# Performance work log

Measured on AMD Instinct MI355X. Metric: run time of the kernel, lower is better.

The kernel has to match this reference:

```python
import jax, jax.numpy as jnp
import numpy as np

N_NODES = 50000
N_EDGES = 800000
IN_F = 96
HID = 64
N_CLS = 32


def setup_inputs() -> dict:
    key = jax.random.key(0)
    k1, k2, k3, k4 = jax.random.split(key, 4)
    x = jax.random.normal(k1, (N_NODES, IN_F), dtype=jnp.float32)
    edge_index = jax.random.randint(k2, (2, N_EDGES), 0, N_NODES, dtype=jnp.int64)
    # xavier_uniform init for weights, zeros for bias
    lim1 = float(np.sqrt(6.0 / (IN_F + HID)))
    lim2 = float(np.sqrt(6.0 / (HID + N_CLS)))
    W1 = jax.random.uniform(k3, (IN_F, HID), minval=-lim1, maxval=lim1, dtype=jnp.float32)
    W2 = jax.random.uniform(k4, (HID, N_CLS), minval=-lim2, maxval=lim2, dtype=jnp.float32)
    b1 = jnp.zeros((HID,), dtype=jnp.float32)
    b2 = jnp.zeros((N_CLS,), dtype=jnp.float32)
    return {"x": x, "edge_index": edge_index, "W1": W1, "b1": b1, "W2": W2, "b2": b2}


def _ghost_conv(h, src, dst, W, b, num_nodes):
    # gather neighbor feats per edge, per-edge matmul, scatter-add, bias
    msg = h[src] @ W                                   # [E, out]
    agg = jax.ops.segment_sum(msg, dst, num_segments=num_nodes)  # [N, out]
    return agg + b


def reference(x, edge_index, W1, b1, W2, b2):
    src, dst = edge_index[0], edge_index[1]
    n = x.shape[0]
    h = jax.nn.relu(_ghost_conv(x, src, dst, W1, b1, n))
    # F.dropout(training=False) is identity in eval mode
    out = _ghost_conv(h, src, dst, W2, b2, n)
    return jax.nn.log_softmax(out, axis=1)
```

## Files before the change

kernel.cpp:

```cpp
#include <hip/hip_runtime.h>
#include <hip/hip_bf16.h>
#include <hip/hip_fp8.h>

typedef __attribute__((ext_vector_type(8))) short bf16x8;
typedef __attribute__((ext_vector_type(4))) float f32x4;

#define NBLK 256
#define NBINS_PAD 800
#define BCAP 2048
#define W1LD 104
#define HLD 72

__device__ inline unsigned short f2bf(float f) {
    unsigned u = __float_as_uint(f);
    return (unsigned short)((u + 0x7fffu + ((u >> 16) & 1u)) >> 16);
}
__device__ inline unsigned pack2(float a, float b) {
    return (unsigned)f2bf(a) | ((unsigned)f2bf(b) << 16);
}
__device__ inline float blo(unsigned u) { return __uint_as_float(u << 16); }
__device__ inline float bhi(unsigned u) { return __uint_as_float(u & 0xffff0000u); }

__device__ inline void acc8(float* a, uint4 v) {
    a[0] += blo(v.x); a[1] += bhi(v.x);
    a[2] += blo(v.y); a[3] += bhi(v.y);
    a[4] += blo(v.z); a[5] += bhi(v.z);
    a[6] += blo(v.w); a[7] += bhi(v.w);
}

__device__ inline void accf8x4(float* a, unsigned u) {
    __hip_fp8_e4m3 t;
    t.__x = (__hip_fp8_storage_t)(u & 0xff);         a[0] += (float)t;
    t.__x = (__hip_fp8_storage_t)((u >> 8) & 0xff);  a[1] += (float)t;
    t.__x = (__hip_fp8_storage_t)((u >> 16) & 0xff); a[2] += (float)t;
    t.__x = (__hip_fp8_storage_t)((u >> 24) & 0xff); a[3] += (float)t;
}
__device__ inline void accf8(float* a, uint4 v) {
    accf8x4(a, v.x); accf8x4(a + 4, v.y); accf8x4(a + 8, v.z); accf8x4(a + 12, v.w);
}

__global__ __launch_bounds__(256) void fused_hist_gemm1(
        const int* __restrict__ ei, int* __restrict__ counts, int E, int chunk, int nb,
        const float* __restrict__ W1, const float* __restrict__ W2,
        unsigned short* __restrict__ w2t,
        const float* __restrict__ X,
        unsigned char* __restrict__ y1f8, int Mtiles) {
    __shared__ int hist[NBINS_PAD];
    __shared__ unsigned short w1l[64 * W1LD];
    int b = blockIdx.x, t = threadIdx.x;
    if (b < NBLK) {
        for (int i = t; i < NBINS_PAD; i += 256) hist[i] = 0;
        __syncthreads();
        int e0 = b * chunk;
        int n = E - e0; if (n > chunk) n = chunk; if (n < 0) n = 0;
        for (int i = t; i < n; i += 256) atomicAdd(&hist[ei[E + e0 + i] >> 6], 1);
        __syncthreads();
        for (int j = t; j < nb; j += 256) counts[j * NBLK + b] = hist[j];
        return;
    }
    if (b == NBLK) {
        for (int idx = t; idx < 64 * 32; idx += 256) {
            int n = idx / 64, k = idx - n * 64;
            w2t[idx] = f2bf(W2[k * 32 + n]);
        }
        return;
    }
    for (int idx = t; idx < 96 * 64; idx += 256) {
        int n = idx / 96, k = idx - n * 96;
        w1l[n * W1LD + k] = f2bf(W1[k * 64 + n]);
    }
    __syncthreads();
    int wave = (b - NBLK - 1) * 4 + (t >> 6);
    if (wave >= Mtiles) return;
    int lane = t & 63;
    int l15 = lane & 15, quad = lane >> 4;
    const float* arow = X + (long)(wave * 16 + l15) * 96 + quad * 8;
    f32x4 acc[4] = {{0,0,0,0},{0,0,0,0},{0,0,0,0},{0,0,0,0}};
#pragma unroll
    for (int tt = 0; tt < 3; ++tt) {
        float4 p0 = *(const float4*)(arow + tt * 32);
        float4 p1 = *(const float4*)(arow + tt * 32 + 4);
        union { bf16x8 v; unsigned u[4]; } a;
        a.u[0] = pack2(p0.x, p0.y); a.u[1] = pack2(p0.z, p0.w);
        a.u[2] = pack2(p1.x, p1.y); a.u[3] = pack2(p1.z, p1.w);
#pragma unroll
        for (int nt = 0; nt < 4; ++nt) {
            bf16x8 bfr = *(const bf16x8*)(w1l + (nt * 16 + l15) * W1LD + tt * 32 + quad * 8);
            acc[nt] = __builtin_amdgcn_mfma_f32_16x16x32_bf16(a.v, bfr, acc[nt], 0, 0, 0);
        }
    }
    int mbase = wave * 16 + quad * 4;
#pragma unroll
    for (int nt = 0; nt < 4; ++nt) {
        int col = nt * 16 + l15;
#pragma unroll
        for (int r = 0; r < 4; ++r) {
            __hip_fp8_e4m3 f(acc[nt][r]);
            y1f8[(long)(mbase + r) * 64 + col] = (unsigned char)f.__x;
        }
    }
}

__global__ __launch_bounds__(256) void rowscan(int* __restrict__ counts,
                                               int* __restrict__ btot, int nb) {
    int w = (blockIdx.x * 256 + threadIdx.x) >> 6;
    int lane = threadIdx.x & 63;
    if (w >= nb) return;
    int* row = counts + (size_t)w * NBLK;
    int c0 = row[lane * 4], c1 = row[lane * 4 + 1];
    int c2 = row[lane * 4 + 2], c3 = row[lane * 4 + 3];
    int sum = c0 + c1 + c2 + c3;
    int s = sum;
#pragma unroll
    for (int o = 1; o < 64; o <<= 1) {
        int tt = __shfl_up(s, o);
        if (lane >= o) s += tt;
    }
    int run = s - sum;
    row[lane * 4] = run;     run += c0;
    row[lane * 4 + 1] = run; run += c1;
    row[lane * 4 + 2] = run; run += c2;
    row[lane * 4 + 3] = run;
    if (lane == 63) btot[w] = s;
}

__global__ __launch_bounds__(256) void blk_place(const int* __restrict__ ei,
                                                 const int* __restrict__ counts,
                                                 unsigned* __restrict__ pairs,
                                                 int E, int chunk, int nb) {
    __shared__ int cur[NBINS_PAD];
    int b = blockIdx.x, t = threadIdx.x;
    for (int j = t; j < nb; j += 256) cur[j] = (j << 11) + counts[j * NBLK + b];
    __syncthreads();
    int e0 = b * chunk;
    int n = E - e0; if (n > chunk) n = chunk; if (n < 0) n = 0;
    for (int i = t; i < n; i += 256) {
        int s = ei[e0 + i], d = ei[E + e0 + i];
        int j = d >> 6;
        int pos = atomicAdd(&cur[j], 1);
        if (pos < ((j + 1) << 11))
            pairs[pos] = (unsigned)s | ((unsigned)(d & 63) << 16);
    }
}

__global__ __launch_bounds__(256) void bucket_fused(
        const unsigned* __restrict__ pairs, const int* __restrict__ btot,
        const uint4* __restrict__ y1f8,
        const float* __restrict__ b1, const unsigned short* __restrict__ w2t,
        int2* __restrict__ noderange, int* __restrict__ srcs,
        unsigned short* __restrict__ y2, int N) {
    __shared__ unsigned spk[BCAP];
    __shared__ int lsrc[BCAP];
    __shared__ int cnt64[64], cur64[64], rs[64], re[64];
    __shared__ unsigned short htile[64 * HLD];
    int b = blockIdx.x, t = threadIdx.x;
    int base = b << 11;
    int cnt = btot[b]; if (cnt > BCAP) cnt = BCAP;
    if (t < 64) cnt64[t] = 0;
    __syncthreads();
    for (int i = t; i < cnt; i += 256) {
        unsigned p = pairs[base + i];
        spk[i] = p;
        atomicAdd(&cnt64[(p >> 16) & 63], 1);
    }
    __syncthreads();
    if (t < 64) {
        int v = cnt64[t], x = v;
#pragma unroll
        for (int o = 1; o < 64; o <<= 1) {
            int y = __shfl_up(x, o);
            if (t >= o) x += y;
        }
        int excl = x - v;
        cur64[t] = excl;
        rs[t] = excl;
        re[t] = excl + v;
        int node = b * 64 + t;
        if (node < N) noderange[node] = make_int2(base + excl, base + excl + v);
    }
    __syncthreads();
    for (int i = t; i < cnt; i += 256) {
        unsigned p = spk[i];
        int pos = atomicAdd(&cur64[(p >> 16) & 63], 1);
        lsrc[pos] = (int)(p & 0xffffu);
    }
    __syncthreads();
    for (int i = t; i < cnt; i += 256) srcs[base + i] = lsrc[i];

    int dl = t >> 2, q = t & 3;
    int s0 = rs[dl], s1 = re[dl];
    float a[16];
#pragma unroll
    for (int i = 0; i < 16; ++i) a[i] = 0.f;
    const uint4* ybase = y1f8 + q;
    int e = s0;
    for (; e + 8 <= s1; e += 8) {
        uint4 u0 = ybase[(long)lsrc[e] * 4],     u1 = ybase[(long)lsrc[e + 1] * 4];
        uint4 u2 = ybase[(long)lsrc[e + 2] * 4], u3 = ybase[(long)lsrc[e + 3] * 4];
        uint4 u4 = ybase[(long)lsrc[e + 4] * 4], u5 = ybase[(long)lsrc[e + 5] * 4];
        uint4 u6 = ybase[(long)lsrc[e + 6] * 4], u7 = ybase[(long)lsrc[e + 7] * 4];
        accf8(a, u0); accf8(a, u1); accf8(a, u2); accf8(a, u3);
        accf8(a, u4); accf8(a, u5); accf8(a, u6); accf8(a, u7);
    }
    for (; e < s1; ++e) accf8(a, ybase[(long)lsrc[e] * 4]);
    {
        const float* bq = b1 + q * 16;
        float v[16];
#pragma unroll
        for (int j = 0; j < 16; ++j) v[j] = fmaxf(a[j] + bq[j], 0.f);
        uint4 o0, o1;
        o0.x = pack2(v[0], v[1]);   o0.y = pack2(v[2], v[3]);
        o0.z = pack2(v[4], v[5]);   o0.w = pack2(v[6], v[7]);
        o1.x = pack2(v[8], v[9]);   o1.y = pack2(v[10], v[11]);
        o1.z = pack2(v[12], v[13]); o1.w = pack2(v[14], v[15]);
        uint4* hp = (uint4*)(htile + dl * HLD + q * 16);
        hp[0] = o0;
        hp[1] = o1;
    }
    __syncthreads();
    int w = t >> 6, lane = t & 63;
    int l15 = lane & 15, quad = lane >> 4;
    const unsigned short* arow = htile + (w * 16 + l15) * HLD + quad * 8;
    f32x4 acc2[2] = {{0,0,0,0},{0,0,0,0}};
#pragma unroll
    for (int t2 = 0; t2 < 2; ++t2) {
        bf16x8 af = *(const bf16x8*)(arow + t2 * 32);
#pragma unroll
        for (int nt = 0; nt < 2; ++nt) {
            bf16x8 bfr = *(const bf16x8*)(w2t + (long)(nt * 16 + l15) * 64 + t2 * 32 + quad * 8);
            acc2[nt] = __builtin_amdgcn_mfma_f32_16x16x32_bf16(af, bfr, acc2[nt], 0, 0, 0);
        }
    }
    int mbase = b * 64 + w * 16 + quad * 4;
#pragma unroll
    for (int nt = 0; nt < 2; ++nt) {
        int col = nt * 16 + l15;
#pragma unroll
        for (int r = 0; r < 4; ++r) {
            int n = mbase + r;
            if (n < N) y2[(long)n * 32 + col] = f2bf(acc2[nt][r]);
        }
    }
}

__global__ void gather_lsm(const uint4* __restrict__ y2, const int2* __restrict__ rng,
                           const int* __restrict__ srcs, const float* __restrict__ bias,
                           float* __restrict__ out, int N) {
    int gid = blockIdx.x * blockDim.x + threadIdx.x;
    int n = gid >> 2;
    if (n >= N) return;
    int q = gid & 3;
    int2 r01 = rng[n];
    int s0 = r01.x, s1 = r01.y;
    float a[8];
#pragma unroll
    for (int i = 0; i < 8; ++i) a[i] = 0.f;
    const uint4* base = y2 + q;
    int e = s0;
    for (; e + 8 <= s1; e += 8) {
        uint4 u0 = base[(long)srcs[e] * 4],     u1 = base[(long)srcs[e + 1] * 4];
        uint4 u2 = base[(long)srcs[e + 2] * 4], u3 = base[(long)srcs[e + 3] * 4];
        uint4 u4 = base[(long)srcs[e + 4] * 4], u5 = base[(long)srcs[e + 5] * 4];
        uint4 u6 = base[(long)srcs[e + 6] * 4], u7 = base[(long)srcs[e + 7] * 4];
        acc8(a, u0); acc8(a, u1); acc8(a, u2); acc8(a, u3);
        acc8(a, u4); acc8(a, u5); acc8(a, u6); acc8(a, u7);
    }
    for (; e < s1; ++e) acc8(a, base[(long)srcs[e] * 4]);
    const float* bq = bias + q * 8;
    float m = -1e30f;
#pragma unroll
    for (int i = 0; i < 8; ++i) { a[i] += bq[i]; m = fmaxf(m, a[i]); }
    m = fmaxf(m, __shfl_xor(m, 1));
    m = fmaxf(m, __shfl_xor(m, 2));
    float s = 0.f;
#pragma unroll
    for (int i = 0; i < 8; ++i) s += __expf(a[i] - m);
    s += __shfl_xor(s, 1);
    s += __shfl_xor(s, 2);
    float ls = m + __logf(s);
    float* op = out + (long)n * 32 + q * 8;
#pragma unroll
    for (int i = 0; i < 8; ++i) op[i] = a[i] - ls;
}

extern "C" void kernel_launch(void* const* d_in, const int* in_sizes, int n_in,
                              void* d_out, int out_size, void* d_ws, size_t ws_size,
                              hipStream_t stream) {
    const float* x  = (const float*)d_in[0];
    const int*   ei = (const int*)d_in[1];
    const float* W1 = (const float*)d_in[2];
    const float* b1 = (const float*)d_in[3];
    const float* W2 = (const float*)d_in[4];
    const float* b2 = (const float*)d_in[5];
    float* out = (float*)d_out;

    const int N = in_sizes[0] / 96;
    const int E = in_sizes[1] / 2;
    const int nb = (N + 63) / 64;
    const int chunk = (E + NBLK - 1) / NBLK;

    char* p = (char*)d_ws;
    unsigned char*  y1f8 = (unsigned char*)p;     p += (size_t)N * 64;
    unsigned short* y2   = (unsigned short*)p;    p += (size_t)N * 32 * 2;
    unsigned short* w2t  = (unsigned short*)p;    p += 64 * 32 * 2;
    int2* noderange = (int2*)p;                   p += (size_t)N * 8;
    int* counts = (int*)p;                        p += ((size_t)nb * NBLK * 4 + 12) & ~15ull;
    int* btot   = (int*)p;                        p += ((size_t)nb * 4 + 12) & ~15ull;
    unsigned* pairs = (unsigned*)p;               p += (size_t)nb * BCAP * 4;
    int* srcs   = (int*)p;                        p += (size_t)nb * BCAP * 4;

    const int Mtiles = N / 16;
    const int gblocks = (Mtiles + 3) / 4;

    fused_hist_gemm1<<<NBLK + 1 + gblocks, 256, 0, stream>>>(
        ei, counts, E, chunk, nb, W1, W2, w2t, x, y1f8, Mtiles);
    rowscan<<<(nb * 64 + 255) / 256, 256, 0, stream>>>(counts, btot, nb);
    blk_place<<<NBLK, 256, 0, stream>>>(ei, counts, pairs, E, chunk, nb);
    bucket_fused<<<nb, 256, 0, stream>>>(pairs, btot, (const uint4*)y1f8,
                                         b1, w2t, noderange, srcs, y2, N);
    gather_lsm<<<(N * 4 + 255) / 256, 256, 0, stream>>>(
        (const uint4*)y2, noderange, srcs, b2, out, N);
}
```

Measured before the change: 142.1 us.

## Fuse all GNN stages into one cooperative persistent kernel with grid syncs

Adds a single cooperative kernel that runs histogram plus GEMM1, row scan, edge placement, bucketed layer-1 aggregation with GEMM2, and layer-2 gather with log-softmax, separated by grid-wide syncs. One block per 64-node bucket replaces the five separate launches. The final stage reuses the per-bucket source lists and node ranges still held in shared memory, so the noderange and srcs arrays are no longer written to or read from global memory. In exchange, every block rebuilds the bf16 W1 tile, the histogram is spread over more blocks, and grid syncs add cost. The old multi-kernel path stays as a fallback if the cooperative launch fails.

```diff
diff --git a/kernel.cpp b/kernel.cpp
--- a/kernel.cpp
+++ b/kernel.cpp
@@ -1,6 +1,9 @@
 #include <hip/hip_runtime.h>
 #include <hip/hip_bf16.h>
 #include <hip/hip_fp8.h>
+#include <hip/hip_cooperative_groups.h>
+
+namespace cg = cooperative_groups;
 
 typedef __attribute__((ext_vector_type(8))) short bf16x8;
 typedef __attribute__((ext_vector_type(4))) float f32x4;
@@ -10,6 +13,7 @@
 #define BCAP 2048
 #define W1LD 104
 #define HLD 72
+#define SMEM_BYTES 26624
 
 __device__ inline unsigned short f2bf(float f) {
     unsigned u = __float_as_uint(f);
@@ -27,7 +31,6 @@
     a[4] += blo(v.z); a[5] += bhi(v.z);
     a[6] += blo(v.w); a[7] += bhi(v.w);
 }
-
 __device__ inline void accf8x4(float* a, unsigned u) {
     __hip_fp8_e4m3 t;
     t.__x = (__hip_fp8_storage_t)(u & 0xff);         a[0] += (float)t;
@@ -39,11 +42,246 @@
     accf8x4(a, v.x); accf8x4(a + 4, v.y); accf8x4(a + 8, v.z); accf8x4(a + 12, v.w);
 }
 
+__global__ __launch_bounds__(256, 4) void mega(
+        const int* __restrict__ ei, int E, int nb, int chunk,
+        const float* __restrict__ W1, const float* __restrict__ W2,
+        unsigned short* __restrict__ w2t,
+        const float* __restrict__ X,
+        const float* __restrict__ b1, const float* __restrict__ b2,
+        unsigned char* __restrict__ y1f8, unsigned short* __restrict__ y2,
+        int* __restrict__ counts, int* __restrict__ btot,
+        unsigned* __restrict__ pairs, float* __restrict__ out,
+        int N, int Mtiles) {
+    cg::grid_group grid = cg::this_grid();
+    __shared__ __align__(16) char smem[SMEM_BYTES];
+    int b = blockIdx.x, t = threadIdx.x;
+
+    {
+        int* hist = (int*)smem;
+        unsigned short* w1l = (unsigned short*)(smem + 8192);
+        for (int i = t; i < NBINS_PAD; i += 256) hist[i] = 0;
+        for (int idx = t; idx < 96 * 64; idx += 256) {
+            int n = idx / 96, k = idx - n * 96;
+            w1l[n * W1LD + k] = f2bf(W1[k * 64 + n]);
+        }
+        if (b == 0) {
+            for (int idx = t; idx < 64 * 32; idx += 256) {
+                int n = idx / 64, k = idx - n * 64;
+                w2t[idx] = f2bf(W2[k * 32 + n]);
+            }
+        }
+        __syncthreads();
+        int e0 = b * chunk;
+        int n = E - e0; if (n > chunk) n = chunk; if (n < 0) n = 0;
+        for (int i = t; i < n; i += 256) atomicAdd(&hist[ei[E + e0 + i] >> 6], 1);
+        int wave = b * 4 + (t >> 6);
+        if (wave < Mtiles) {
+            int lane = t & 63;
+            int l15 = lane & 15, quad = lane >> 4;
+            const float* arow = X + (long)(wave * 16 + l15) * 96 + quad * 8;
+            f32x4 acc[4] = {{0,0,0,0},{0,0,0,0},{0,0,0,0},{0,0,0,0}};
+#pragma unroll
+            for (int tt = 0; tt < 3; ++tt) {
+                float4 p0 = *(const float4*)(arow + tt * 32);
+                float4 p1 = *(const float4*)(arow + tt * 32 + 4);
+                union { bf16x8 v; unsigned u[4]; } a;
+                a.u[0] = pack2(p0.x, p0.y); a.u[1] = pack2(p0.z, p0.w);
+                a.u[2] = pack2(p1.x, p1.y); a.u[3] = pack2(p1.z, p1.w);
+#pragma unroll
+                for (int nt = 0; nt < 4; ++nt) {
+                    bf16x8 bfr = *(const bf16x8*)(w1l + (nt * 16 + l15) * W1LD + tt * 32 + quad * 8);
+                    acc[nt] = __builtin_amdgcn_mfma_f32_16x16x32_bf16(a.v, bfr, acc[nt], 0, 0, 0);
+                }
+            }
+            int mbase = wave * 16 + quad * 4;
+#pragma unroll
+            for (int nt = 0; nt < 4; ++nt) {
+                int col = nt * 16 + l15;
+#pragma unroll
+                for (int r = 0; r < 4; ++r) {
+                    __hip_fp8_e4m3 f(acc[nt][r]);
+                    y1f8[(long)(mbase + r) * 64 + col] = (unsigned char)f.__x;
+                }
+            }
+        }
+        __syncthreads();
+        for (int j = t; j < nb; j += 256) counts[(size_t)j * nb + b] = hist[j];
+    }
+    grid.sync();
+
+    {
+        if (t < 64) {
+            int* row = counts + (size_t)b * nb;
+            int CPL = (nb + 63) >> 6;
+            int lo = t * CPL; if (lo > nb) lo = nb;
+            int hi = lo + CPL; if (hi > nb) hi = nb;
+            int lsum = 0;
+            for (int i = lo; i < hi; ++i) lsum += row[i];
+            int s = lsum;
+#pragma unroll
+            for (int o = 1; o < 64; o <<= 1) {
+                int tt2 = __shfl_up(s, o);
+                if (t >= o) s += tt2;
+            }
+            int run = s - lsum;
+            for (int i = lo; i < hi; ++i) { int c = row[i]; row[i] = run; run += c; }
+            if (t == 63) btot[b] = s;
+        }
+    }
+    grid.sync();
+
+    {
+        int* cur = (int*)smem;
+        for (int j = t; j < nb; j += 256) cur[j] = (j << 11) + counts[(size_t)j * nb + b];
+        __syncthreads();
+        int e0 = b * chunk;
+        int n = E - e0; if (n > chunk) n = chunk; if (n < 0) n = 0;
+        for (int i = t; i < n; i += 256) {
+            int s = ei[e0 + i], d = ei[E + e0 + i];
+            int j = d >> 6;
+            int pos = atomicAdd(&cur[j], 1);
+            if (pos < ((j + 1) << 11))
+                pairs[pos] = (unsigned)s | ((unsigned)(d & 63) << 16);
+        }
+    }
+    grid.sync();
+
+    unsigned* spk = (unsigned*)smem;
+    int* lsrc  = (int*)(smem + 8192);
+    int* cnt64 = (int*)(smem + 16384);
+    int* cur64 = (int*)(smem + 16640);
+    int* rs    = (int*)(smem + 16896);
+    int* re    = (int*)(smem + 17152);
+    unsigned short* htile = (unsigned short*)(smem + 17408);
+    {
+        int base = b << 11;
+        int cnt = btot[b]; if (cnt > BCAP) cnt = BCAP;
+        if (t < 64) cnt64[t] = 0;
+        __syncthreads();
+        for (int i = t; i < cnt; i += 256) {
+            unsigned p = pairs[base + i];
+            spk[i] = p;
+            atomicAdd(&cnt64[(p >> 16) & 63], 1);
+        }
+        __syncthreads();
+        if (t < 64) {
+            int v = cnt64[t], x = v;
+#pragma unroll
+            for (int o = 1; o < 64; o <<= 1) {
+                int y = __shfl_up(x, o);
+                if (t >= o) x += y;
+            }
+            int excl = x - v;
+            cur64[t] = excl;
+            rs[t] = excl;
+            re[t] = excl + v;
+        }
+        __syncthreads();
+        for (int i = t; i < cnt; i += 256) {
+            unsigned p = spk[i];
+            int pos = atomicAdd(&cur64[(p >> 16) & 63], 1);
+            lsrc[pos] = (int)(p & 0xffffu);
+        }
+        __syncthreads();
+        int dl = t >> 2, q = t & 3;
+        int s0 = rs[dl], s1 = re[dl];
+        float a[16];
+#pragma unroll
+        for (int i = 0; i < 16; ++i) a[i] = 0.f;
+        const uint4* ybase = (const uint4*)y1f8 + q;
+        int e = s0;
+        for (; e + 8 <= s1; e += 8) {
+            uint4 u0 = ybase[(long)lsrc[e] * 4],     u1 = ybase[(long)lsrc[e + 1] * 4];
+            uint4 u2 = ybase[(long)lsrc[e + 2] * 4], u3 = ybase[(long)lsrc[e + 3] * 4];
+            uint4 u4 = ybase[(long)lsrc[e + 4] * 4], u5 = ybase[(long)lsrc[e + 5] * 4];
+            uint4 u6 = ybase[(long)lsrc[e + 6] * 4], u7 = ybase[(long)lsrc[e + 7] * 4];
+            accf8(a, u0); accf8(a, u1); accf8(a, u2); accf8(a, u3);
+            accf8(a, u4); accf8(a, u5); accf8(a, u6); accf8(a, u7);
+        }
+        for (; e < s1; ++e) accf8(a, ybase[(long)lsrc[e] * 4]);
+        {
+            const float* bq = b1 + q * 16;
+            float v[16];
+#pragma unroll
+            for (int j = 0; j < 16; ++j) v[j] = fmaxf(a[j] + bq[j], 0.f);
+            uint4 o0, o1;
+            o0.x = pack2(v[0], v[1]);   o0.y = pack2(v[2], v[3]);
+            o0.z = pack2(v[4], v[5]);   o0.w = pack2(v[6], v[7]);
+            o1.x = pack2(v[8], v[9]);   o1.y = pack2(v[10], v[11]);
+            o1.z = pack2(v[12], v[13]); o1.w = pack2(v[14], v[15]);
+            uint4* hp = (uint4*)(htile + dl * HLD + q * 16);
+            hp[0] = o0;
+            hp[1] = o1;
+        }
+        __syncthreads();
+        int w = t >> 6, lane = t & 63;
+        int l15 = lane & 15, quad = lane >> 4;
+        const unsigned short* arow = htile + (w * 16 + l15) * HLD + quad * 8;
+        f32x4 acc2[2] = {{0,0,0,0},{0,0,0,0}};
+#pragma unroll
+        for (int t2 = 0; t2 < 2; ++t2) {
+            bf16x8 af = *(const bf16x8*)(arow + t2 * 32);
+#pragma unroll
+            for (int nt = 0; nt < 2; ++nt) {
+                bf16x8 bfr = *(const bf16x8*)(w2t + (long)(nt * 16 + l15) * 64 + t2 * 32 + quad * 8);
+                acc2[nt] = __builtin_amdgcn_mfma_f32_16x16x32_bf16(af, bfr, acc2[nt], 0, 0, 0);
+            }
+        }
+        int mbase = b * 64 + w * 16 + quad * 4;
+#pragma unroll
+        for (int nt = 0; nt < 2; ++nt) {
+            int col = nt * 16 + l15;
+#pragma unroll
+            for (int r = 0; r < 4; ++r) {
+                int n = mbase + r;
+                if (n < N) y2[(long)n * 32 + col] = f2bf(acc2[nt][r]);
+            }
+        }
+    }
+    grid.sync();
+
+    {
+        int dl = t >> 2, q = t & 3;
+        int node = b * 64 + dl;
+        if (node < N) {
+            int s0 = rs[dl], s1 = re[dl];
+            float a[8];
+#pragma unroll
+            for (int i = 0; i < 8; ++i) a[i] = 0.f;
+            const uint4* base = (const uint4*)y2 + q;
+            int e = s0;
+            for (; e + 8 <= s1; e += 8) {
+                uint4 u0 = base[(long)lsrc[e] * 4],     u1 = base[(long)lsrc[e + 1] * 4];
+                uint4 u2 = base[(long)lsrc[e + 2] * 4], u3 = base[(long)lsrc[e + 3] * 4];
+                uint4 u4 = base[(long)lsrc[e + 4] * 4], u5 = base[(long)lsrc[e + 5] * 4];
+                uint4 u6 = base[(long)lsrc[e + 6] * 4], u7 = base[(long)lsrc[e + 7] * 4];
+                acc8(a, u0); acc8(a, u1); acc8(a, u2); acc8(a, u3);
+                acc8(a, u4); acc8(a, u5); acc8(a, u6); acc8(a, u7);
+            }
+            for (; e < s1; ++e) acc8(a, base[(long)lsrc[e] * 4]);
+            const float* bq = b2 + q * 8;
+            float m = -1e30f;
+#pragma unroll
+            for (int i = 0; i < 8; ++i) { a[i] += bq[i]; m = fmaxf(m, a[i]); }
+            m = fmaxf(m, __shfl_xor(m, 1));
+            m = fmaxf(m, __shfl_xor(m, 2));
+            float s = 0.f;
+#pragma unroll
+            for (int i = 0; i < 8; ++i) s += __expf(a[i] - m);
+            s += __shfl_xor(s, 1);
+            s += __shfl_xor(s, 2);
+            float ls = m + __logf(s);
+            float* op = out + (long)node * 32 + q * 8;
+#pragma unroll
+            for (int i = 0; i < 8; ++i) op[i] = a[i] - ls;
+        }
+    }
+}
+
 __global__ __launch_bounds__(256) void fused_hist_gemm1(
         const int* __restrict__ ei, int* __restrict__ counts, int E, int chunk, int nb,
         const float* __restrict__ W1, const float* __restrict__ W2,
-        unsigned short* __restrict__ w2t,
-        const float* __restrict__ X,
+        unsigned short* __restrict__ w2t, const float* __restrict__ X,
         unsigned char* __restrict__ y1f8, int Mtiles) {
     __shared__ int hist[NBINS_PAD];
     __shared__ unsigned short w1l[64 * W1LD];
@@ -145,10 +383,9 @@
 
 __global__ __launch_bounds__(256) void bucket_fused(
         const unsigned* __restrict__ pairs, const int* __restrict__ btot,
-        const uint4* __restrict__ y1f8,
-        const float* __restrict__ b1, const unsigned short* __restrict__ w2t,
-        int2* __restrict__ noderange, int* __restrict__ srcs,
-        unsigned short* __restrict__ y2, int N) {
+        const uint4* __restrict__ y1f8, const float* __restrict__ b1,
+        const unsigned short* __restrict__ w2t, int2* __restrict__ noderange,
+        int* __restrict__ srcs, unsigned short* __restrict__ y2, int N) {
     __shared__ unsigned spk[BCAP];
     __shared__ int lsrc[BCAP];
     __shared__ int cnt64[64], cur64[64], rs[64], re[64];
@@ -172,9 +409,7 @@
             if (t >= o) x += y;
         }
         int excl = x - v;
-        cur64[t] = excl;
-        rs[t] = excl;
-        re[t] = excl + v;
+        cur64[t] = excl; rs[t] = excl; re[t] = excl + v;
         int node = b * 64 + t;
         if (node < N) noderange[node] = make_int2(base + excl, base + excl + v);
     }
@@ -186,7 +421,6 @@
     }
     __syncthreads();
     for (int i = t; i < cnt; i += 256) srcs[base + i] = lsrc[i];
-
     int dl = t >> 2, q = t & 3;
     int s0 = rs[dl], s1 = re[dl];
     float a[16];
@@ -214,8 +448,7 @@
         o1.x = pack2(v[8], v[9]);   o1.y = pack2(v[10], v[11]);
         o1.z = pack2(v[12], v[13]); o1.w = pack2(v[14], v[15]);
         uint4* hp = (uint4*)(htile + dl * HLD + q * 16);
-        hp[0] = o0;
-        hp[1] = o1;
+        hp[0] = o0; hp[1] = o1;
     }
     __syncthreads();
     int w = t >> 6, lane = t & 63;
@@ -297,25 +530,38 @@
     const int N = in_sizes[0] / 96;
     const int E = in_sizes[1] / 2;
     const int nb = (N + 63) / 64;
-    const int chunk = (E + NBLK - 1) / NBLK;
 
     char* p = (char*)d_ws;
     unsigned char*  y1f8 = (unsigned char*)p;     p += (size_t)N * 64;
     unsigned short* y2   = (unsigned short*)p;    p += (size_t)N * 32 * 2;
     unsigned short* w2t  = (unsigned short*)p;    p += 64 * 32 * 2;
     int2* noderange = (int2*)p;                   p += (size_t)N * 8;
-    int* counts = (int*)p;                        p += ((size_t)nb * NBLK * 4 + 12) & ~15ull;
+    int* counts = (int*)p;                        p += ((size_t)nb * nb * 4 + 12) & ~15ull;
     int* btot   = (int*)p;                        p += ((size_t)nb * 4 + 12) & ~15ull;
     unsigned* pairs = (unsigned*)p;               p += (size_t)nb * BCAP * 4;
     int* srcs   = (int*)p;                        p += (size_t)nb * BCAP * 4;
 
     const int Mtiles = N / 16;
+
+    {
+        int Ep = E, nbp = nb, Np = N, Mt = Mtiles;
+        int chunkC = (E + nb - 1) / nb;
+        void* args[] = { (void*)&ei, &Ep, &nbp, &chunkC, (void*)&W1, (void*)&W2,
+                         (void*)&w2t, (void*)&x, (void*)&b1, (void*)&b2,
+                         (void*)&y1f8, (void*)&y2, (void*)&counts, (void*)&btot,
+                         (void*)&pairs, (void*)&out, &Np, &Mt };
+        hipError_t err = hipLaunchCooperativeKernel((void*)mega, dim3(nb), dim3(256),
+                                                    args, 0, stream);
+        if (err == hipSuccess) return;
+        (void)hipGetLastError();
+    }
+
+    const int chunkF = (E + NBLK - 1) / NBLK;
     const int gblocks = (Mtiles + 3) / 4;
-
     fused_hist_gemm1<<<NBLK + 1 + gblocks, 256, 0, stream>>>(
-        ei, counts, E, chunk, nb, W1, W2, w2t, x, y1f8, Mtiles);
+        ei, counts, E, chunkF, nb, W1, W2, w2t, x, y1f8, Mtiles);
     rowscan<<<(nb * 64 + 255) / 256, 256, 0, stream>>>(counts, btot, nb);
-    blk_place<<<NBLK, 256, 0, stream>>>(ei, counts, pairs, E, chunk, nb);
+    blk_place<<<NBLK, 256, 0, stream>>>(ei, counts, pairs, E, chunkF, nb);
     bucket_fused<<<nb, 256, 0, stream>>>(pairs, btot, (const uint4*)y1f8,
                                          b1, w2t, noderange, srcs, y2, N);
     gather_lsm<<<(N * 4 + 255) / 256, 256, 0, stream>>>(
```

New measurement: 567.0 us. +299.1%, slower.
